# Kernel tuning notes

Measured on AMD Instinct MI355X. Metric: run time of the kernel, lower is better.

The kernel has to match this reference:

```python
import jax, jax.numpy as jnp
import numpy as np


def _mab(Q, K, wq, bq, wk, bk, wv, bv, wo, bo, num_heads):
    # Faithful MAB (no LayerNorm: ln=False throughout SetPooler's settrans).
    V = wq.shape[1]
    dh = V // num_heads
    q = Q @ wq + bq          # [..., Sq, V]
    k = K @ wk + bk          # [..., Sk, V]
    v = K @ wv + bv
    def heads(x):
        return x.reshape(*x.shape[:-1], num_heads, dh).swapaxes(-2, -3)  # [..., h, S, dh]
    qh, kh, vh = heads(q), heads(k), heads(v)
    scale = jnp.asarray(1.0 / np.sqrt(V), q.dtype)  # note: torch code scales by sqrt(dim_V), not sqrt(head_dim)
    A = jax.nn.softmax(jnp.einsum('...hqd,...hkd->...hqk', qh, kh) * scale, axis=-1)
    O = qh + jnp.einsum('...hqk,...hkd->...hqd', A, vh)               # residual on Q_
    O = O.swapaxes(-2, -3).reshape(*Q.shape[:-1], V)                  # merge heads back
    return O + jax.nn.relu(O @ wo + bo)


def _forward(rep_R, GA,
             sab0_wq, sab0_bq, sab0_wk, sab0_bk, sab0_wv, sab0_bv, sab0_wo, sab0_bo,
             sab1_wq, sab1_bq, sab1_wk, sab1_bk, sab1_wv, sab1_bv, sab1_wo, sab1_bo,
             pma_S, pma_wq, pma_bq, pma_wk, pma_bk, pma_wv, pma_bv, pma_wo, pma_bo,
             mlp_w1, mlp_b1, mlp_w2, mlp_b2, mlp_w3, mlp_b3):
    # masked mul: GA [G,N] -> [1,G,N,1] broadcast against rep_R [B,G,N,D]
    X = GA[None, :, :, None] * rep_R
    # two SABs (self-attention), 4 heads each
    X = _mab(X, X, sab0_wq, sab0_bq, sab0_wk, sab0_bk, sab0_wv, sab0_bv, sab0_wo, sab0_bo, 4)
    X = _mab(X, X, sab1_wq, sab1_bq, sab1_wk, sab1_bk, sab1_wv, sab1_bv, sab1_wo, sab1_bo, 4)
    # PMA: 1 learned seed, 2 heads, squeeze_out
    S = jnp.broadcast_to(pma_S, (*X.shape[:-2], *pma_S.shape))  # [B,G,1,D]
    O = _mab(S, X, pma_wq, pma_bq, pma_wk, pma_bk, pma_wv, pma_bv, pma_wo, pma_bo, 2)
    O = O[..., 0, :]  # squeeze_out -> [B,G,D]
    # MLP head: D -> 512 -> 512 -> 2*dim_z
    h = jax.nn.relu(O @ mlp_w1 + mlp_b1)
    h = jax.nn.relu(h @ mlp_w2 + mlp_b2)
    return h @ mlp_w3 + mlp_b3


def setup_inputs() -> dict:
    key = jax.random.key(0)
    B, G, N, D = 4, 16, 512, 256
    dz2 = 256  # 2 * dim_z
    ks = iter(jax.random.split(key, 64))
    def lin(fi, fo):
        w = jax.random.normal(next(ks), (fi, fo), jnp.float32) / np.float32(np.sqrt(fi))
        return w, jnp.zeros((fo,), jnp.float32)
    inp = {}
    inp['rep_R'] = jax.random.normal(next(ks), (B, G, N, D), jnp.float32)
    inp['GA'] = jax.random.uniform(next(ks), (G, N), jnp.float32)
    for i in range(2):
        for nm in ('q', 'k', 'v', 'o'):
            w, b = lin(D, D)
            inp[f'sab{i}_w{nm}'] = w
            inp[f'sab{i}_b{nm}'] = b
    inp['pma_S'] = jax.random.normal(next(ks), (1, D), jnp.float32) * np.float32(np.sqrt(6.0 / (1 + D)))
    for nm in ('q', 'k', 'v', 'o'):
        w, b = lin(D, D)
        inp[f'pma_w{nm}'] = w
        inp[f'pma_b{nm}'] = b
    inp['mlp_w1'], inp['mlp_b1'] = lin(D, 512)
    inp['mlp_w2'], inp['mlp_b2'] = lin(512, 512)
    inp['mlp_w3'], inp['mlp_b3'] = lin(512, dz2)
    return inp


def reference(rep_R, GA,
              sab0_wq, sab0_bq, sab0_wk, sab0_bk, sab0_wv, sab0_bv, sab0_wo, sab0_bo,
              sab1_wq, sab1_bq, sab1_wk, sab1_bk, sab1_wv, sab1_bv, sab1_wo, sab1_bo,
              pma_S, pma_wq, pma_bq, pma_wk, pma_bk, pma_wv, pma_bv, pma_wo, pma_bo,
              mlp_w1, mlp_b1, mlp_w2, mlp_b2, mlp_w3, mlp_b3):
    return _forward(rep_R, GA,
                    sab0_wq, sab0_bq, sab0_wk, sab0_bk, sab0_wv, sab0_bv, sab0_wo, sab0_bo,
                    sab1_wq, sab1_bq, sab1_wk, sab1_bk, sab1_wv, sab1_bv, sab1_wo, sab1_bo,
                    pma_S, pma_wq, pma_bq, pma_wk, pma_bk, pma_wv, pma_bv, pma_wo, pma_bo,
                    mlp_w1, mlp_b1, mlp_w2, mlp_b2, mlp_w3, mlp_b3)
```

## Files before the change

kernel.cpp:

```cpp
#include <hip/hip_runtime.h>
#include <hip/hip_bf16.h>

typedef __attribute__((ext_vector_type(4))) float  f32x4;
typedef __attribute__((ext_vector_type(8))) __bf16 bf16x8;
typedef __attribute__((ext_vector_type(4))) __bf16 bf16x4;

#define LOG2E_O16 0.09016844005556021f

__device__ __forceinline__ void gload_lds16(const void* g, void* l) {
  __builtin_amdgcn_global_load_lds(
      (const __attribute__((address_space(1))) void*)g,
      (__attribute__((address_space(3))) void*)l, 16, 0, 0);
}

__global__ __launch_bounds__(256) void scale_kernel(
    const float* __restrict__ rep, const float* __restrict__ GA, __bf16* __restrict__ X)
{
  size_t i = (size_t)blockIdx.x * 256 + threadIdx.x;
  size_t e = i * 4;
  f32x4 r = *(const f32x4*)(rep + e);
  int dn = (int)(e >> 8);
  int n  = dn & 511;
  int g  = (dn >> 9) & 15;
  float ga = GA[g * 512 + n];
  bf16x4 o;
  o[0] = (__bf16)(r[0] * ga); o[1] = (__bf16)(r[1] * ga);
  o[2] = (__bf16)(r[2] * ga); o[3] = (__bf16)(r[3] * ga);
  *(bf16x4*)(X + e) = o;
}

struct WPtrs { const float* w[10]; };
__global__ __launch_bounds__(256) void wconv_kernel(WPtrs ws, __bf16* __restrict__ out)
{
  __shared__ float t[64][65];
  const float* w = ws.w[blockIdx.y];
  __bf16* o = out + (size_t)blockIdx.y * 65536;
  const int tr = (blockIdx.x & 3) * 64, tc = (blockIdx.x >> 2) * 64;
  const int r4 = threadIdx.x >> 6, c = threadIdx.x & 63;
#pragma unroll
  for (int p = 0; p < 16; ++p) {
    int row = p * 4 + r4;
    t[row][c] = w[(size_t)(tr + row) * 256 + tc + c];
  }
  __syncthreads();
#pragma unroll
  for (int p = 0; p < 16; ++p) {
    int row = p * 4 + r4;
    o[(size_t)(tc + row) * 256 + tr + c] = (__bf16)t[c][row];
  }
}

struct QKV3 {
  const __bf16* Bt[3];
  const float* bias[3];
  __bf16* out[3];
};

template<int NW>
__global__ __launch_bounds__(256) void gemmqkv_kernel(
    const __bf16* __restrict__ A, QKV3 args, int K)
{
  __shared__ __align__(16) __bf16 sA[128 * 32];
  __shared__ __align__(16) __bf16 sB[128 * 32];
  const int tid = threadIdx.x, lane = tid & 63, wv = tid >> 6;
  const int l16 = lane & 15, lg = lane >> 4;
  const int wr = (wv >> 1) * 64, wc = (wv & 1) * 64;

  const int nblk = gridDim.x, cpx = nblk >> 3, orig = blockIdx.x;
  const int wg  = (orig & 7) * cpx + (orig >> 3);
  const int r   = wg / (2 * NW), rem = wg % (2 * NW);
  const int j   = rem >> 1;
  const int bm  = r * 128, bn = (rem & 1) * 128;
  const __bf16* __restrict__ Bt = args.Bt[j];

  const int row_s = tid >> 2;
  const int kb_s  = (tid & 3) * 16;

  f32x4 acc[4][4] = {};

  for (int k0 = 0; k0 < K; k0 += 32) {
#pragma unroll
    for (int rr = 0; rr < 2; ++rr) {
      int row = rr * 64 + row_s;
      int kb  = kb_s ^ (((row >> 1) & 3) << 4);
      const char* gA = (const char*)(A  + (size_t)(bm + row) * K + k0) + kb;
      const char* gB = (const char*)(Bt + (size_t)(bn + row) * K + k0) + kb;
      char* dA = (char*)sA + rr * 4096 + wv * 1024;
      char* dB = (char*)sB + rr * 4096 + wv * 1024;
      gload_lds16(gA, dA);
      gload_lds16(gB, dB);
    }
    __syncthreads();
    bf16x8 af[4], bfr[4];
#pragma unroll
    for (int mi = 0; mi < 4; ++mi) {
      int row = wr + mi * 16 + l16;
      int kb = (lg << 4) ^ (((row >> 1) & 3) << 4);
      af[mi] = *(const bf16x8*)((const char*)sA + row * 64 + kb);
    }
#pragma unroll
    for (int ni = 0; ni < 4; ++ni) {
      int row = wc + ni * 16 + l16;
      int kb = (lg << 4) ^ (((row >> 1) & 3) << 4);
      bfr[ni] = *(const bf16x8*)((const char*)sB + row * 64 + kb);
    }
#pragma unroll
    for (int mi = 0; mi < 4; ++mi)
#pragma unroll
      for (int ni = 0; ni < 4; ++ni)
        acc[mi][ni] = __builtin_amdgcn_mfma_f32_16x16x32_bf16(af[mi], bfr[ni], acc[mi][ni], 0, 0, 0);
    __syncthreads();
  }

  const float* bias = args.bias[j];
  __bf16* C = args.out[j];
#pragma unroll
  for (int mi = 0; mi < 4; ++mi)
#pragma unroll
    for (int ni = 0; ni < 4; ++ni) {
      int col = bn + wc + ni * 16 + l16;
      float bval = bias[col];
      int row0 = bm + wr + mi * 16 + lg * 4;
#pragma unroll
      for (int i = 0; i < 4; ++i) {
        int row = row0 + i;
        C[(size_t)row * 256 + col] = (__bf16)(acc[mi][ni][i] + bval);
      }
    }
}

__global__ __launch_bounds__(256) void gemm128_kernel(
    const __bf16* __restrict__ A, const __bf16* __restrict__ Bt,
    const float* __restrict__ bias, const __bf16* __restrict__ R,
    __bf16* __restrict__ C, int K)
{
  __shared__ __align__(16) __bf16 sA[128 * 32];
  __shared__ __align__(16) __bf16 sB[128 * 32];
  const int tid = threadIdx.x, lane = tid & 63, wv = tid >> 6;
  const int l16 = lane & 15, lg = lane >> 4;
  const int wr = (wv >> 1) * 64, wc = (wv & 1) * 64;

  const int nblk = gridDim.x, cpx = nblk >> 3, orig = blockIdx.x;
  const int wg  = (orig & 7) * cpx + (orig >> 3);
  const int bm  = (wg >> 1) * 128, bn = (wg & 1) * 128;

  const int row_s = tid >> 2;
  const int kb_s  = (tid & 3) * 16;

  f32x4 acc[4][4] = {};

  for (int k0 = 0; k0 < K; k0 += 32) {
#pragma unroll
    for (int rr = 0; rr < 2; ++rr) {
      int row = rr * 64 + row_s;
      int kb  = kb_s ^ (((row >> 1) & 3) << 4);
      const char* gA = (const char*)(A  + (size_t)(bm + row) * K + k0) + kb;
      const char* gB = (const char*)(Bt + (size_t)(bn + row) * K + k0) + kb;
      char* dA = (char*)sA + rr * 4096 + wv * 1024;
      char* dB = (char*)sB + rr * 4096 + wv * 1024;
      gload_lds16(gA, dA);
      gload_lds16(gB, dB);
    }
    __syncthreads();
    bf16x8 af[4], bfr[4];
#pragma unroll
    for (int mi = 0; mi < 4; ++mi) {
      int row = wr + mi * 16 + l16;
      int kb = (lg << 4) ^ (((row >> 1) & 3) << 4);
      af[mi] = *(const bf16x8*)((const char*)sA + row * 64 + kb);
    }
#pragma unroll
    for (int ni = 0; ni < 4; ++ni) {
      int row = wc + ni * 16 + l16;
      int kb = (lg << 4) ^ (((row >> 1) & 3) << 4);
      bfr[ni] = *(const bf16x8*)((const char*)sB + row * 64 + kb);
    }
#pragma unroll
    for (int mi = 0; mi < 4; ++mi)
#pragma unroll
      for (int ni = 0; ni < 4; ++ni)
        acc[mi][ni] = __builtin_amdgcn_mfma_f32_16x16x32_bf16(af[mi], bfr[ni], acc[mi][ni], 0, 0, 0);
    __syncthreads();
  }

#pragma unroll
  for (int mi = 0; mi < 4; ++mi)
#pragma unroll
    for (int ni = 0; ni < 4; ++ni) {
      int col = bn + wc + ni * 16 + l16;
      float bval = bias[col];
      int row0 = bm + wr + mi * 16 + lg * 4;
#pragma unroll
      for (int i = 0; i < 4; ++i) {
        int row = row0 + i;
        float v = fmaxf(acc[mi][ni][i] + bval, 0.f);
        C[(size_t)row * 256 + col] = (__bf16)((float)R[(size_t)row * 256 + col] + v);
      }
    }
}

template<int EPI, bool OUTF32>
__global__ __launch_bounds__(256) void gemm_kernel(
    const __bf16* __restrict__ A, const float* __restrict__ B,
    const float* __restrict__ bias, const __bf16* __restrict__ R,
    void* __restrict__ Cv, int M, int N, int K)
{
  __shared__ __bf16 sA[64][40];
  __shared__ __bf16 sB[64][40];
  const int tid  = threadIdx.x;
  const int lane = tid & 63;
  const int wv   = tid >> 6;
  const int wr   = (wv >> 1) * 32;
  const int wc   = (wv & 1) * 32;
  const int bm   = blockIdx.x * 64;
  const int bn   = blockIdx.y * 64;
  const int l16  = lane & 15;
  const int lk8  = (lane >> 4) * 8;

  const int a_r = tid >> 2, a_c = (tid & 3) * 8;
  const int b_c = tid & 63, b_k = (tid >> 6) * 8;

  f32x4 acc[2][2] = {};

  for (int k0 = 0; k0 < K; k0 += 32) {
    bf16x8 av = *(const bf16x8*)(A + (size_t)(bm + a_r) * K + k0 + a_c);
    float bvf[8];
#pragma unroll
    for (int j = 0; j < 8; ++j)
      bvf[j] = B[(size_t)(k0 + b_k + j) * N + bn + b_c];
    *(bf16x8*)&sA[a_r][a_c] = av;
    bf16x8 bb;
#pragma unroll
    for (int j = 0; j < 8; ++j) bb[j] = (__bf16)bvf[j];
    *(bf16x8*)&sB[b_c][b_k] = bb;
    __syncthreads();
    bf16x8 af0 = *(const bf16x8*)&sA[wr + l16][lk8];
    bf16x8 af1 = *(const bf16x8*)&sA[wr + 16 + l16][lk8];
    bf16x8 bf0 = *(const bf16x8*)&sB[wc + l16][lk8];
    bf16x8 bf1 = *(const bf16x8*)&sB[wc + 16 + l16][lk8];
    acc[0][0] = __builtin_amdgcn_mfma_f32_16x16x32_bf16(af0, bf0, acc[0][0], 0, 0, 0);
    acc[0][1] = __builtin_amdgcn_mfma_f32_16x16x32_bf16(af0, bf1, acc[0][1], 0, 0, 0);
    acc[1][0] = __builtin_amdgcn_mfma_f32_16x16x32_bf16(af1, bf0, acc[1][0], 0, 0, 0);
    acc[1][1] = __builtin_amdgcn_mfma_f32_16x16x32_bf16(af1, bf1, acc[1][1], 0, 0, 0);
    __syncthreads();
  }

#pragma unroll
  for (int mi = 0; mi < 2; ++mi)
#pragma unroll
    for (int ni = 0; ni < 2; ++ni) {
      int col = bn + wc + ni * 16 + l16;
      float bval = bias[col];
      int row0 = bm + wr + mi * 16 + (lane >> 4) * 4;
#pragma unroll
      for (int i = 0; i < 4; ++i) {
        int row = row0 + i;
        float v = acc[mi][ni][i] + bval;
        if (EPI == 1) v = fmaxf(v, 0.f);
        if (EPI == 2) v = (float)R[(size_t)row * N + col] + fmaxf(v, 0.f);
        if (OUTF32) ((float*)Cv)[(size_t)row * N + col] = v;
        else        ((__bf16*)Cv)[(size_t)row * N + col] = (__bf16)v;
      }
    }
}

__global__ __launch_bounds__(512, 2) void attn_sab_kernel(
    __bf16* __restrict__ Q, const __bf16* __restrict__ Kb, const __bf16* __restrict__ Vb)
{
  __shared__ __align__(16) __bf16 sK[128][72];
  __shared__ __align__(16) __bf16 sV[64][136];
  __shared__ __align__(16) __bf16 sP[8][16][72];

  const int orig = blockIdx.x;
  const int wg   = (orig & 7) * 64 + (orig >> 3);
  const int qh   = wg & 1;
  const int pair = wg >> 1;
  const int head = pair & 3;
  const int item = pair >> 2;

  const int tid  = threadIdx.x;
  const int lane = tid & 63;
  const int wv   = tid >> 6;
  const int l16  = lane & 15;
  const int lg   = lane >> 4;
  const size_t base = (size_t)item * (512 * 256) + (size_t)head * 64;
  const int qrow0 = qh * 256 + wv * 32;

  bf16x8 aq[2][2];
#pragma unroll
  for (int qb = 0; qb < 2; ++qb) {
    const size_t qrow = base + (size_t)(qrow0 + qb * 16 + l16) * 256;
    aq[qb][0] = *(const bf16x8*)(Q + qrow + lg * 8);
    aq[qb][1] = *(const bf16x8*)(Q + qrow + 32 + lg * 8);
  }

  f32x4 acco[2][4] = {};
  float lsum[2] = {0.f, 0.f};

  const int kr  = tid >> 3, kc8 = (tid & 7) * 8;
  const int vch = tid & 63, vk8 = (tid >> 6) * 8;

  bf16x8 kreg[2], vreg[2];

#define LOADC(cc) do {                                                             \
    _Pragma("unroll")                                                              \
    for (int p = 0; p < 2; ++p) {                                                  \
      kreg[p] = *(const bf16x8*)(Kb + base + (size_t)((cc)*128 + p*64 + kr)*256 + kc8); \
      bf16x8 vv;                                                                   \
      _Pragma("unroll")                                                            \
      for (int jj = 0; jj < 8; ++jj)                                               \
        vv[jj] = Vb[base + (size_t)((cc)*128 + p*64 + vk8 + jj)*256 + vch];        \
      vreg[p] = vv;                                                                \
    } } while (0)

  LOADC(0);

  for (int c = 0; c < 4; ++c) {
    if (c) __syncthreads();
#pragma unroll
    for (int p = 0; p < 2; ++p) {
      *(bf16x8*)&sK[p * 64 + kr][kc8] = kreg[p];
      *(bf16x8*)&sV[vch][p * 64 + vk8] = vreg[p];
    }
    __syncthreads();
    if (c < 3) LOADC(c + 1);

#pragma unroll
    for (int qb = 0; qb < 2; ++qb) {
#pragma unroll
      for (int half = 0; half < 2; ++half) {
        f32x4 s[4];
#pragma unroll
        for (int st = 0; st < 4; ++st) {
          int krl = half * 64 + st * 16 + l16;
          f32x4 z = {};
          s[st] = __builtin_amdgcn_mfma_f32_16x16x32_bf16(
                      *(const bf16x8*)&sK[krl][lg * 8], aq[qb][0], z, 0, 0, 0);
        }
#pragma unroll
        for (int st = 0; st < 4; ++st) {
          int krl = half * 64 + st * 16 + l16;
          s[st] = __builtin_amdgcn_mfma_f32_16x16x32_bf16(
                      *(const bf16x8*)&sK[krl][32 + lg * 8], aq[qb][1], s[st], 0, 0, 0);
        }
#pragma unroll
        for (int st = 0; st < 4; ++st) {
          bf16x4 pv4;
          float ls = 0.f;
#pragma unroll
          for (int i = 0; i < 4; ++i) {
            float p = __builtin_amdgcn_exp2f(s[st][i] * LOG2E_O16);
            ls += p;
            pv4[i] = (__bf16)p;
          }
          lsum[qb] += ls;
          *(bf16x4*)&sP[wv][l16][st * 16 + lg * 4] = pv4;
        }
#pragma unroll
        for (int kk = 0; kk < 2; ++kk) {
          bf16x8 ap = *(const bf16x8*)&sP[wv][l16][kk * 32 + lg * 8];
#pragma unroll
          for (int vt = 0; vt < 4; ++vt) {
            bf16x8 bvv = *(const bf16x8*)&sV[vt * 16 + l16][half * 64 + kk * 32 + lg * 8];
            acco[qb][vt] = __builtin_amdgcn_mfma_f32_16x16x32_bf16(ap, bvv, acco[qb][vt], 0, 0, 0);
          }
        }
      }
    }
  }
#undef LOADC

#pragma unroll
  for (int qb = 0; qb < 2; ++qb) {
    float t = lsum[qb];
    t += __shfl_xor(t, 16, 64);
    t += __shfl_xor(t, 32, 64);
#pragma unroll
    for (int i = 0; i < 4; ++i) {
      float tot = __shfl(t, lg * 4 + i, 64);
      float inv = 1.0f / tot;
      int row = qrow0 + qb * 16 + lg * 4 + i;
#pragma unroll
      for (int vt = 0; vt < 4; ++vt) {
        size_t idx = base + (size_t)row * 256 + vt * 16 + l16;
        Q[idx] = (__bf16)((float)Q[idx] + acco[qb][vt][i] * inv);
      }
    }
  }
}

__global__ __launch_bounds__(256) void pma_q_kernel(
    const float* __restrict__ S, const float* __restrict__ wq,
    const float* __restrict__ bq, float* __restrict__ qout)
{
  __shared__ float sS[256];
  int t = threadIdx.x;
  sS[t] = S[t];
  __syncthreads();
  float acc = bq[t];
  for (int k = 0; k < 256; ++k) acc += sS[k] * wq[k * 256 + t];
  qout[t] = acc;
}

__global__ __launch_bounds__(256) void pma_attn_kernel(
    const float* __restrict__ qpma, const __bf16* __restrict__ Kb,
    const __bf16* __restrict__ Vb, __bf16* __restrict__ Opma)
{
  __shared__ float sq[256];
  __shared__ float sP[1024];
  __shared__ float red[256];
  __shared__ float sl[2];
  const int item = blockIdx.x;
  const int t = threadIdx.x;
  sq[t] = qpma[t];
  __syncthreads();

#pragma unroll
  for (int rep = 0; rep < 4; ++rep) {
    int task = rep * 256 + t;
    int h = task >> 9, key = task & 511;
    const __bf16* kr = Kb + ((size_t)item * 512 + key) * 256 + h * 128;
    float s = 0.f;
#pragma unroll
    for (int d8 = 0; d8 < 128; d8 += 8) {
      bf16x8 kv = *(const bf16x8*)(kr + d8);
#pragma unroll
      for (int j = 0; j < 8; ++j) s += sq[h * 128 + d8 + j] * (float)kv[j];
    }
    sP[task] = __builtin_amdgcn_exp2f(s * LOG2E_O16);
  }
  __syncthreads();
  {
    int h = t >> 7, kb = t & 127;
    float p = 0.f;
#pragma unroll
    for (int j = 0; j < 4; ++j) p += sP[h * 512 + kb + j * 128];
    red[t] = p;
  }
  __syncthreads();
  if (t < 2) {
    float s = 0.f;
    for (int i = 0; i < 128; ++i) s += red[t * 128 + i];
    sl[t] = 1.f / s;
  }
  __syncthreads();
  {
    int h = t >> 7;
    float acc = 0.f;
    for (int key = 0; key < 512; ++key)
      acc += sP[h * 512 + key] * (float)Vb[((size_t)item * 512 + key) * 256 + t];
    Opma[item * 256 + t] = (__bf16)(sq[t] + acc * sl[h]);
  }
}

extern "C" void kernel_launch(void* const* d_in, const int* in_sizes, int n_in,
                              void* d_out, int out_size, void* d_ws, size_t ws_size,
                              hipStream_t stream)
{
  const size_t XSZ = (size_t)64 * 512 * 256;
  if (ws_size < 4 * XSZ * sizeof(__bf16) + (4u << 20)) return;

  const float* rep = (const float*)d_in[0];
  const float* GA  = (const float*)d_in[1];

  __bf16* X    = (__bf16*)d_ws;
  __bf16* Qb   = X  + XSZ;
  __bf16* Kb   = Qb + XSZ;
  __bf16* Vb   = Kb + XSZ;
  __bf16* wT   = Vb + XSZ;
  float*  qpma = (float*)(wT + 10 * 65536);
  __bf16* Opma = (__bf16*)(qpma + 256);
  __bf16* O2   = Opma + 64 * 256;
  __bf16* H1   = O2 + 64 * 256;
  __bf16* H2   = H1 + 64 * 512;

  WPtrs wp;
  for (int s = 0; s < 2; ++s)
    for (int j = 0; j < 4; ++j)
      wp.w[s * 4 + j] = (const float*)d_in[2 + s * 8 + j * 2];
  wp.w[8] = (const float*)d_in[21];
  wp.w[9] = (const float*)d_in[23];
  wconv_kernel<<<dim3(16, 10), 256, 0, stream>>>(wp, wT);

  scale_kernel<<<8192, 256, 0, stream>>>(rep, GA, X);

  for (int sab = 0; sab < 2; ++sab) {
    QKV3 a;
    a.Bt[0] = wT + (size_t)(sab * 4 + 0) * 65536;
    a.Bt[1] = wT + (size_t)(sab * 4 + 1) * 65536;
    a.Bt[2] = wT + (size_t)(sab * 4 + 2) * 65536;
    a.bias[0] = (const float*)d_in[2 + sab * 8 + 1];
    a.bias[1] = (const float*)d_in[2 + sab * 8 + 3];
    a.bias[2] = (const float*)d_in[2 + sab * 8 + 5];
    a.out[0] = Qb; a.out[1] = Kb; a.out[2] = Vb;
    gemmqkv_kernel<3><<<1536, 256, 0, stream>>>(X, a, 256);
    attn_sab_kernel<<<512, 512, 0, stream>>>(Qb, Kb, Vb);
    gemm128_kernel<<<512, 256, 0, stream>>>(Qb, wT + (size_t)(sab * 4 + 3) * 65536,
        (const float*)d_in[2 + sab * 8 + 7], Qb, X, 256);
  }

  pma_q_kernel<<<1, 256, 0, stream>>>((const float*)d_in[18], (const float*)d_in[19],
                                      (const float*)d_in[20], qpma);
  {
    QKV3 a;
    a.Bt[0] = wT + (size_t)8 * 65536;
    a.Bt[1] = wT + (size_t)9 * 65536;
    a.Bt[2] = wT;
    a.bias[0] = (const float*)d_in[22];
    a.bias[1] = (const float*)d_in[24];
    a.bias[2] = (const float*)d_in[22];
    a.out[0] = Kb; a.out[1] = Vb; a.out[2] = Kb;
    gemmqkv_kernel<2><<<1024, 256, 0, stream>>>(X, a, 256);
  }
  pma_attn_kernel<<<64, 256, 0, stream>>>(qpma, Kb, Vb, Opma);
  gemm_kernel<2, false><<<dim3(1, 4), 256, 0, stream>>>(Opma, (const float*)d_in[25],
      (const float*)d_in[26], Opma, O2, 64, 256, 256);
  gemm_kernel<1, false><<<dim3(1, 8), 256, 0, stream>>>(O2, (const float*)d_in[27],
      (const float*)d_in[28], nullptr, H1, 64, 512, 256);
  gemm_kernel<1, false><<<dim3(1, 8), 256, 0, stream>>>(H1, (const float*)d_in[29],
      (const float*)d_in[30], nullptr, H2, 64, 512, 512);
  gemm_kernel<0, true><<<dim3(1, 4), 256, 0, stream>>>(H2, (const float*)d_in[31],
      (const float*)d_in[32], nullptr, (float*)d_out, 64, 256, 512);
}
```

Baseline: 248.1 us.

## Use 32x32 MFMA with register-resident P in SAB attention; deepen GEMM K-step

```diff
diff --git a/kernel.cpp b/kernel.cpp
--- a/kernel.cpp
+++ b/kernel.cpp
@@ -1,9 +1,12 @@
 #include <hip/hip_runtime.h>
 #include <hip/hip_bf16.h>
 
-typedef __attribute__((ext_vector_type(4))) float  f32x4;
-typedef __attribute__((ext_vector_type(8))) __bf16 bf16x8;
-typedef __attribute__((ext_vector_type(4))) __bf16 bf16x4;
+typedef __attribute__((ext_vector_type(4)))  float  f32x4;
+typedef __attribute__((ext_vector_type(16))) float  f32x16;
+typedef __attribute__((ext_vector_type(8)))  __bf16 bf16x8;
+typedef __attribute__((ext_vector_type(4)))  __bf16 bf16x4;
+typedef unsigned int u32x2 __attribute__((ext_vector_type(2)));
+typedef unsigned int u32x4 __attribute__((ext_vector_type(4)));
 
 #define LOG2E_O16 0.09016844005556021f
 
@@ -11,6 +14,17 @@
   __builtin_amdgcn_global_load_lds(
       (const __attribute__((address_space(1))) void*)g,
       (__attribute__((address_space(3))) void*)l, 16, 0, 0);
+}
+
+__device__ __forceinline__ void pl32swap(unsigned int& a, unsigned int& b) {
+  u32x2 r = __builtin_amdgcn_permlane32_swap(a, b, false, false);
+  a = r[0]; b = r[1];
+}
+
+__device__ __forceinline__ unsigned int pack2bf(float a, float b) {
+  unsigned short ua = __builtin_bit_cast(unsigned short, (__bf16)a);
+  unsigned short ub = __builtin_bit_cast(unsigned short, (__bf16)b);
+  return (unsigned int)ua | ((unsigned int)ub << 16);
 }
 
 __global__ __launch_bounds__(256) void scale_kernel(
@@ -50,6 +64,49 @@
   }
 }
 
+#define GEMM64_BODY(A_, B_, bmv, bnv, Kv)                                          \
+  f32x4 acc[4][4] = {};                                                            \
+  for (int k0 = 0; k0 < (Kv); k0 += 64) {                                          \
+    _Pragma("unroll")                                                              \
+    for (int r = 0; r < 4; ++r) {                                                  \
+      int rowl = r * 32 + (tid >> 3);                                              \
+      int sl = (tid & 7) ^ (rowl & 7);                                             \
+      gload_lds16((const char*)((A_) + (size_t)((bmv) + rowl) * (Kv) + k0) + sl * 16, \
+                  (char*)sA + r * 4096 + wv * 1024);                               \
+      gload_lds16((const char*)((B_) + (size_t)((bnv) + rowl) * (Kv) + k0) + sl * 16, \
+                  (char*)sB + r * 4096 + wv * 1024);                               \
+    }                                                                              \
+    __syncthreads();                                                               \
+    bf16x8 af[4][2], bfr[4][2];                                                    \
+    _Pragma("unroll")                                                              \
+    for (int mi = 0; mi < 4; ++mi) {                                               \
+      int row = wr + mi * 16 + l16;                                                \
+      _Pragma("unroll")                                                            \
+      for (int kk = 0; kk < 2; ++kk) {                                             \
+        int sl = (kk * 4 + lg) ^ (row & 7);                                        \
+        af[mi][kk] = *(const bf16x8*)((const char*)sA + row * 128 + sl * 16);      \
+      }                                                                            \
+    }                                                                              \
+    _Pragma("unroll")                                                              \
+    for (int ni = 0; ni < 4; ++ni) {                                               \
+      int row = wc + ni * 16 + l16;                                                \
+      _Pragma("unroll")                                                            \
+      for (int kk = 0; kk < 2; ++kk) {                                             \
+        int sl = (kk * 4 + lg) ^ (row & 7);                                        \
+        bfr[ni][kk] = *(const bf16x8*)((const char*)sB + row * 128 + sl * 16);     \
+      }                                                                            \
+    }                                                                              \
+    _Pragma("unroll")                                                              \
+    for (int kk = 0; kk < 2; ++kk)                                                 \
+      _Pragma("unroll")                                                            \
+      for (int mi = 0; mi < 4; ++mi)                                               \
+        _Pragma("unroll")                                                          \
+        for (int ni = 0; ni < 4; ++ni)                                             \
+          acc[mi][ni] = __builtin_amdgcn_mfma_f32_16x16x32_bf16(                   \
+              af[mi][kk], bfr[ni][kk], acc[mi][ni], 0, 0, 0);                      \
+    __syncthreads();                                                               \
+  }
+
 struct QKV3 {
   const __bf16* Bt[3];
   const float* bias[3];
@@ -60,57 +117,20 @@
 __global__ __launch_bounds__(256) void gemmqkv_kernel(
     const __bf16* __restrict__ A, QKV3 args, int K)
 {
-  __shared__ __align__(16) __bf16 sA[128 * 32];
-  __shared__ __align__(16) __bf16 sB[128 * 32];
+  __shared__ __align__(16) __bf16 sA[128 * 64];
+  __shared__ __align__(16) __bf16 sB[128 * 64];
   const int tid = threadIdx.x, lane = tid & 63, wv = tid >> 6;
   const int l16 = lane & 15, lg = lane >> 4;
   const int wr = (wv >> 1) * 64, wc = (wv & 1) * 64;
 
   const int nblk = gridDim.x, cpx = nblk >> 3, orig = blockIdx.x;
   const int wg  = (orig & 7) * cpx + (orig >> 3);
-  const int r   = wg / (2 * NW), rem = wg % (2 * NW);
+  const int r_  = wg / (2 * NW), rem = wg % (2 * NW);
   const int j   = rem >> 1;
-  const int bm  = r * 128, bn = (rem & 1) * 128;
+  const int bm  = r_ * 128, bn = (rem & 1) * 128;
   const __bf16* __restrict__ Bt = args.Bt[j];
 
-  const int row_s = tid >> 2;
-  const int kb_s  = (tid & 3) * 16;
-
-  f32x4 acc[4][4] = {};
-
-  for (int k0 = 0; k0 < K; k0 += 32) {
-#pragma unroll
-    for (int rr = 0; rr < 2; ++rr) {
-      int row = rr * 64 + row_s;
-      int kb  = kb_s ^ (((row >> 1) & 3) << 4);
-      const char* gA = (const char*)(A  + (size_t)(bm + row) * K + k0) + kb;
-      const char* gB = (const char*)(Bt + (size_t)(bn + row) * K + k0) + kb;
-      char* dA = (char*)sA + rr * 4096 + wv * 1024;
-      char* dB = (char*)sB + rr * 4096 + wv * 1024;
-      gload_lds16(gA, dA);
-      gload_lds16(gB, dB);
-    }
-    __syncthreads();
-    bf16x8 af[4], bfr[4];
-#pragma unroll
-    for (int mi = 0; mi < 4; ++mi) {
-      int row = wr + mi * 16 + l16;
-      int kb = (lg << 4) ^ (((row >> 1) & 3) << 4);
-      af[mi] = *(const bf16x8*)((const char*)sA + row * 64 + kb);
-    }
-#pragma unroll
-    for (int ni = 0; ni < 4; ++ni) {
-      int row = wc + ni * 16 + l16;
-      int kb = (lg << 4) ^ (((row >> 1) & 3) << 4);
-      bfr[ni] = *(const bf16x8*)((const char*)sB + row * 64 + kb);
-    }
-#pragma unroll
-    for (int mi = 0; mi < 4; ++mi)
-#pragma unroll
-      for (int ni = 0; ni < 4; ++ni)
-        acc[mi][ni] = __builtin_amdgcn_mfma_f32_16x16x32_bf16(af[mi], bfr[ni], acc[mi][ni], 0, 0, 0);
-    __syncthreads();
-  }
+  GEMM64_BODY(A, Bt, bm, bn, K)
 
   const float* bias = args.bias[j];
   __bf16* C = args.out[j];
@@ -122,10 +142,8 @@
       float bval = bias[col];
       int row0 = bm + wr + mi * 16 + lg * 4;
 #pragma unroll
-      for (int i = 0; i < 4; ++i) {
-        int row = row0 + i;
-        C[(size_t)row * 256 + col] = (__bf16)(acc[mi][ni][i] + bval);
-      }
+      for (int i = 0; i < 4; ++i)
+        C[(size_t)(row0 + i) * 256 + col] = (__bf16)(acc[mi][ni][i] + bval);
     }
 }
 
@@ -134,8 +152,8 @@
     const float* __restrict__ bias, const __bf16* __restrict__ R,
     __bf16* __restrict__ C, int K)
 {
-  __shared__ __align__(16) __bf16 sA[128 * 32];
-  __shared__ __align__(16) __bf16 sB[128 * 32];
+  __shared__ __align__(16) __bf16 sA[128 * 64];
+  __shared__ __align__(16) __bf16 sB[128 * 64];
   const int tid = threadIdx.x, lane = tid & 63, wv = tid >> 6;
   const int l16 = lane & 15, lg = lane >> 4;
   const int wr = (wv >> 1) * 64, wc = (wv & 1) * 64;
@@ -144,44 +162,7 @@
   const int wg  = (orig & 7) * cpx + (orig >> 3);
   const int bm  = (wg >> 1) * 128, bn = (wg & 1) * 128;
 
-  const int row_s = tid >> 2;
-  const int kb_s  = (tid & 3) * 16;
-
-  f32x4 acc[4][4] = {};
-
-  for (int k0 = 0; k0 < K; k0 += 32) {
-#pragma unroll
-    for (int rr = 0; rr < 2; ++rr) {
-      int row = rr * 64 + row_s;
-      int kb  = kb_s ^ (((row >> 1) & 3) << 4);
-      const char* gA = (const char*)(A  + (size_t)(bm + row) * K + k0) + kb;
-      const char* gB = (const char*)(Bt + (size_t)(bn + row) * K + k0) + kb;
-      char* dA = (char*)sA + rr * 4096 + wv * 1024;
-      char* dB = (char*)sB + rr * 4096 + wv * 1024;
-      gload_lds16(gA, dA);
-      gload_lds16(gB, dB);
-    }
-    __syncthreads();
-    bf16x8 af[4], bfr[4];
-#pragma unroll
-    for (int mi = 0; mi < 4; ++mi) {
-      int row = wr + mi * 16 + l16;
-      int kb = (lg << 4) ^ (((row >> 1) & 3) << 4);
-      af[mi] = *(const bf16x8*)((const char*)sA + row * 64 + kb);
-    }
-#pragma unroll
-    for (int ni = 0; ni < 4; ++ni) {
-      int row = wc + ni * 16 + l16;
-      int kb = (lg << 4) ^ (((row >> 1) & 3) << 4);
-      bfr[ni] = *(const bf16x8*)((const char*)sB + row * 64 + kb);
-    }
-#pragma unroll
-    for (int mi = 0; mi < 4; ++mi)
-#pragma unroll
-      for (int ni = 0; ni < 4; ++ni)
-        acc[mi][ni] = __builtin_amdgcn_mfma_f32_16x16x32_bf16(af[mi], bfr[ni], acc[mi][ni], 0, 0, 0);
-    __syncthreads();
-  }
+  GEMM64_BODY(A, Bt, bm, bn, K)
 
 #pragma unroll
   for (int mi = 0; mi < 4; ++mi)
@@ -269,48 +250,41 @@
 {
   __shared__ __align__(16) __bf16 sK[128][72];
   __shared__ __align__(16) __bf16 sV[64][136];
-  __shared__ __align__(16) __bf16 sP[8][16][72];
-
-  const int orig = blockIdx.x;
-  const int wg   = (orig & 7) * 64 + (orig >> 3);
-  const int qh   = wg & 1;
-  const int pair = wg >> 1;
-  const int head = pair & 3;
-  const int item = pair >> 2;
-
+
+  const int head = blockIdx.x & 3;
+  const int item = blockIdx.x >> 2;
   const int tid  = threadIdx.x;
   const int lane = tid & 63;
   const int wv   = tid >> 6;
-  const int l16  = lane & 15;
-  const int lg   = lane >> 4;
+  const int l32  = lane & 31;
+  const int hg   = lane >> 5;
   const size_t base = (size_t)item * (512 * 256) + (size_t)head * 64;
-  const int qrow0 = qh * 256 + wv * 32;
-
-  bf16x8 aq[2][2];
-#pragma unroll
-  for (int qb = 0; qb < 2; ++qb) {
-    const size_t qrow = base + (size_t)(qrow0 + qb * 16 + l16) * 256;
-    aq[qb][0] = *(const bf16x8*)(Q + qrow + lg * 8);
-    aq[qb][1] = *(const bf16x8*)(Q + qrow + 32 + lg * 8);
-  }
-
-  f32x4 acco[2][4] = {};
+  const int qr0 = wv * 64;
+
+  bf16x8 bq[2][4];
+#pragma unroll
+  for (int qb = 0; qb < 2; ++qb)
+#pragma unroll
+    for (int ks = 0; ks < 4; ++ks)
+      bq[qb][ks] = *(const bf16x8*)(Q + base + (size_t)(qr0 + qb * 32 + l32) * 256
+                                    + ks * 16 + hg * 8);
+
+  f32x16 acco[2][2] = {};
   float lsum[2] = {0.f, 0.f};
 
   const int kr  = tid >> 3, kc8 = (tid & 7) * 8;
-  const int vch = tid & 63, vk8 = (tid >> 6) * 8;
+  const int vch = tid & 63, vk8 = wv * 8;
 
   bf16x8 kreg[2], vreg[2];
-
-#define LOADC(cc) do {                                                             \
-    _Pragma("unroll")                                                              \
-    for (int p = 0; p < 2; ++p) {                                                  \
+#define LOADC(cc) do {                                                                  \
+    _Pragma("unroll")                                                                   \
+    for (int p = 0; p < 2; ++p) {                                                       \
       kreg[p] = *(const bf16x8*)(Kb + base + (size_t)((cc)*128 + p*64 + kr)*256 + kc8); \
-      bf16x8 vv;                                                                   \
-      _Pragma("unroll")                                                            \
-      for (int jj = 0; jj < 8; ++jj)                                               \
-        vv[jj] = Vb[base + (size_t)((cc)*128 + p*64 + vk8 + jj)*256 + vch];        \
-      vreg[p] = vv;                                                                \
+      bf16x8 vv;                                                                        \
+      _Pragma("unroll")                                                                 \
+      for (int jj = 0; jj < 8; ++jj)                                                    \
+        vv[jj] = Vb[base + (size_t)((cc)*128 + p*64 + vk8 + jj)*256 + vch];             \
+      vreg[p] = vv;                                                                     \
     } } while (0)
 
   LOADC(0);
@@ -326,45 +300,47 @@
     if (c < 3) LOADC(c + 1);
 
 #pragma unroll
-    for (int qb = 0; qb < 2; ++qb) {
-#pragma unroll
-      for (int half = 0; half < 2; ++half) {
-        f32x4 s[4];
-#pragma unroll
-        for (int st = 0; st < 4; ++st) {
-          int krl = half * 64 + st * 16 + l16;
-          f32x4 z = {};
-          s[st] = __builtin_amdgcn_mfma_f32_16x16x32_bf16(
-                      *(const bf16x8*)&sK[krl][lg * 8], aq[qb][0], z, 0, 0, 0);
+    for (int st = 0; st < 4; ++st) {
+      bf16x8 kf[4];
+#pragma unroll
+      for (int ks = 0; ks < 4; ++ks)
+        kf[ks] = *(const bf16x8*)&sK[st * 32 + l32][ks * 16 + hg * 8];
+      bf16x8 vf[2][2];
+#pragma unroll
+      for (int ds = 0; ds < 2; ++ds)
+#pragma unroll
+        for (int h = 0; h < 2; ++h)
+          vf[ds][h] = *(const bf16x8*)&sV[ds * 32 + l32][st * 32 + h * 16 + hg * 8];
+
+#pragma unroll
+      for (int qb = 0; qb < 2; ++qb) {
+        f32x16 s = {};
+#pragma unroll
+        for (int ks = 0; ks < 4; ++ks)
+          s = __builtin_amdgcn_mfma_f32_32x32x16_bf16(kf[ks], bq[qb][ks], s, 0, 0, 0);
+
+        unsigned int pk[8];
+        float ls = 0.f;
+#pragma unroll
+        for (int m = 0; m < 8; ++m) {
+          float p0 = __builtin_amdgcn_exp2f(s[2 * m]     * LOG2E_O16);
+          float p1 = __builtin_amdgcn_exp2f(s[2 * m + 1] * LOG2E_O16);
+          ls += p0 + p1;
+          pk[m] = pack2bf(p0, p1);
         }
-#pragma unroll
-        for (int st = 0; st < 4; ++st) {
-          int krl = half * 64 + st * 16 + l16;
-          s[st] = __builtin_amdgcn_mfma_f32_16x16x32_bf16(
-                      *(const bf16x8*)&sK[krl][32 + lg * 8], aq[qb][1], s[st], 0, 0, 0);
-        }
-#pragma unroll
-        for (int st = 0; st < 4; ++st) {
-          bf16x4 pv4;
-          float ls = 0.f;
-#pragma unroll
-          for (int i = 0; i < 4; ++i) {
-            float p = __builtin_amdgcn_exp2f(s[st][i] * LOG2E_O16);
-            ls += p;
-            pv4[i] = (__bf16)p;
-          }
-          lsum[qb] += ls;
-          *(bf16x4*)&sP[wv][l16][st * 16 + lg * 4] = pv4;
-        }
-#pragma unroll
-        for (int kk = 0; kk < 2; ++kk) {
-          bf16x8 ap = *(const bf16x8*)&sP[wv][l16][kk * 32 + lg * 8];
-#pragma unroll
-          for (int vt = 0; vt < 4; ++vt) {
-            bf16x8 bvv = *(const bf16x8*)&sV[vt * 16 + l16][half * 64 + kk * 32 + lg * 8];
-            acco[qb][vt] = __builtin_amdgcn_mfma_f32_16x16x32_bf16(ap, bvv, acco[qb][vt], 0, 0, 0);
-          }
-        }
+        lsum[qb] += ls;
+
+        pl32swap(pk[0], pk[2]); pl32swap(pk[1], pk[3]);
+        pl32swap(pk[4], pk[6]); pl32swap(pk[5], pk[7]);
+        u32x4 b0i = {pk[0], pk[1], pk[2], pk[3]};
+        u32x4 b1i = {pk[4], pk[5], pk[6], pk[7]};
+        bf16x8 pb0 = __builtin_bit_cast(bf16x8, b0i);
+        bf16x8 pb1 = __builtin_bit_cast(bf16x8, b1i);
+
+        acco[qb][0] = __builtin_amdgcn_mfma_f32_32x32x16_bf16(vf[0][0], pb0, acco[qb][0], 0, 0, 0);
+        acco[qb][0] = __builtin_amdgcn_mfma_f32_32x32x16_bf16(vf[0][1], pb1, acco[qb][0], 0, 0, 0);
+        acco[qb][1] = __builtin_amdgcn_mfma_f32_32x32x16_bf16(vf[1][0], pb0, acco[qb][1], 0, 0, 0);
+        acco[qb][1] = __builtin_amdgcn_mfma_f32_32x32x16_bf16(vf[1][1], pb1, acco[qb][1], 0, 0, 0);
       }
     }
   }
@@ -372,20 +348,21 @@
 
 #pragma unroll
   for (int qb = 0; qb < 2; ++qb) {
-    float t = lsum[qb];
-    t += __shfl_xor(t, 16, 64);
-    t += __shfl_xor(t, 32, 64);
-#pragma unroll
-    for (int i = 0; i < 4; ++i) {
-      float tot = __shfl(t, lg * 4 + i, 64);
-      float inv = 1.0f / tot;
-      int row = qrow0 + qb * 16 + lg * 4 + i;
-#pragma unroll
-      for (int vt = 0; vt < 4; ++vt) {
-        size_t idx = base + (size_t)row * 256 + vt * 16 + l16;
-        Q[idx] = (__bf16)((float)Q[idx] + acco[qb][vt][i] * inv);
+    float tot = lsum[qb] + __shfl_xor(lsum[qb], 32, 64);
+    float inv = 1.0f / tot;
+    const size_t qrow = base + (size_t)(qr0 + qb * 32 + l32) * 256;
+#pragma unroll
+    for (int ds = 0; ds < 2; ++ds)
+#pragma unroll
+      for (int rq = 0; rq < 4; ++rq) {
+        int d = ds * 32 + rq * 8 + hg * 4;
+        bf16x4 rv = *(const bf16x4*)(Q + qrow + d);
+        bf16x4 ov;
+#pragma unroll
+        for (int i = 0; i < 4; ++i)
+          ov[i] = (__bf16)((float)rv[i] + acco[qb][ds][rq * 4 + i] * inv);
+        *(bf16x4*)(Q + qrow + d) = ov;
       }
-    }
   }
 }
 
@@ -494,7 +471,7 @@
     a.bias[2] = (const float*)d_in[2 + sab * 8 + 5];
     a.out[0] = Qb; a.out[1] = Kb; a.out[2] = Vb;
     gemmqkv_kernel<3><<<1536, 256, 0, stream>>>(X, a, 256);
-    attn_sab_kernel<<<512, 512, 0, stream>>>(Qb, Kb, Vb);
+    attn_sab_kernel<<<256, 512, 0, stream>>>(Qb, Kb, Vb);
     gemm128_kernel<<<512, 256, 0, stream>>>(Qb, wT + (size_t)(sab * 4 + 3) * 65536,
         (const float*)d_in[2 + sab * 8 + 7], Qb, X, 256);
   }
```

New measurement: 270.1 us. 8.9% more time.
